# Performance work log

Measured on AMD Instinct MI355X. Metric: run time of the kernel, lower is better.

The kernel has to match this reference:

```python
import jax, jax.numpy as jnp
import numpy as np

B, S, A, H, E = 8192, 256, 64, 1024, 8
IN = S + A
OUT = S + 1


def setup_inputs() -> dict:
    key = jax.random.key(0)
    ks = jax.random.split(key, 8)
    state = jax.random.normal(ks[0], (B, S), dtype=jnp.float32)
    action = jax.random.normal(ks[1], (B, A), dtype=jnp.float32)
    idx = jax.random.randint(ks[2], (B,), 0, E, dtype=jnp.int32)
    # Kaiming-ish scaling to keep activations sane
    W1 = jax.random.normal(ks[3], (E, IN, H), dtype=jnp.float32) / np.sqrt(IN)
    b1 = jnp.zeros((E, H), dtype=jnp.float32)
    W2 = jax.random.normal(ks[4], (E, H, H), dtype=jnp.float32) / np.sqrt(H)
    b2 = jnp.zeros((E, H), dtype=jnp.float32)
    W3 = jax.random.normal(ks[5], (E, H, OUT), dtype=jnp.float32) / np.sqrt(H)
    b3 = jnp.zeros((E, OUT), dtype=jnp.float32)
    return {"state": state, "action": action, "idx": idx,
            "W1": W1, "b1": b1, "W2": W2, "b2": b2, "W3": W3, "b3": b3}


def reference(state, action, idx, W1, b1, W2, b2, W3, b3):
    # Dense-MoE style: run all E experts on the full batch, then select the
    # per-sample expert output chosen by idx (matches masked gather/scatter
    # in the torch predict loop).
    x = jnp.concatenate([state, action], axis=-1)                  # [B, IN]
    h = jax.nn.relu(jnp.einsum('bi,eih->beh', x, W1) + b1)         # [B, E, H]
    h = jax.nn.relu(jnp.einsum('beh,ehk->bek', h, W2) + b2)        # [B, E, H]
    out = jnp.einsum('beh,eho->beo', h, W3) + b3                   # [B, E, S+1]
    sel = jnp.take_along_axis(out, idx[:, None, None], axis=1)[:, 0]  # [B, S+1]
    s_dim = state.shape[-1]
    delta = sel[:, :s_dim]
    reward = sel[:, s_dim:]
    next_state = state + delta
    return next_state, reward
```

## Files before the change

### kernel.cpp

```cpp
#include <hip/hip_runtime.h>
#include <stdint.h>

#define B_SZ   8192
#define IN_DIM 320
#define H_DIM  1024
#define E_NUM  8
#define OUT_DIM 257
#define MAXT1  72
#define MAXT2  136

typedef __bf16 bf16x8 __attribute__((ext_vector_type(8)));
typedef float  f32x4  __attribute__((ext_vector_type(4)));

typedef unsigned int __attribute__((address_space(1))) as1_uint;
typedef unsigned int __attribute__((address_space(3))) as3_uint;

__device__ __forceinline__ void gload_lds16(const void* g, void* l) {
    __builtin_amdgcn_global_load_lds((const as1_uint*)g, (as3_uint*)l, 16, 0, 0);
}

__device__ __forceinline__ unsigned short f2bf(float f) {
    unsigned int u = __float_as_uint(f);
    return (unsigned short)((u + 0x7fffu + ((u >> 16) & 1u)) >> 16);
}

__device__ __forceinline__ void transpose_tiles(
    char* smem, int e, int nt, int kt0, int nkt,
    int K, int Nsrc, int dstRows, bool vec,
    const float* __restrict__ src, unsigned short* __restrict__ dst) {
    unsigned short (*tileU)[65] = (unsigned short(*)[65])smem;
    int tid = threadIdx.x;
    const float* s = src + (size_t)e * K * Nsrc;
    unsigned short* d = dst + (size_t)e * dstRows * K;
    int c4 = (tid & 15) * 4;
    int rb = tid >> 4;
    int n0 = nt * 64;
    for (int kt = kt0; kt < kt0 + nkt; kt++) {
        int k0 = kt * 64;
#pragma unroll
        for (int p = 0; p < 4; p++) {
            int r = rb + p * 16;
            const float* sp = s + (size_t)(k0 + r) * Nsrc + n0 + c4;
            float4 v;
            if (vec) v = *(const float4*)sp;
            else { v.x = sp[0]; v.y = sp[1]; v.z = sp[2]; v.w = sp[3]; }
            tileU[r][c4 + 0] = f2bf(v.x);
            tileU[r][c4 + 1] = f2bf(v.y);
            tileU[r][c4 + 2] = f2bf(v.z);
            tileU[r][c4 + 3] = f2bf(v.w);
        }
        __syncthreads();
#pragma unroll
        for (int p = 0; p < 4; p++) {
            int n = rb + p * 16;
            ushort4 o;
            o.x = tileU[c4 + 0][n];
            o.y = tileU[c4 + 1][n];
            o.z = tileU[c4 + 2][n];
            o.w = tileU[c4 + 3][n];
            *(ushort4*)&d[(size_t)(n0 + n) * K + k0 + c4] = o;
        }
        __syncthreads();
    }
}

__device__ __forceinline__ void prep_bucket(
    char* smem, const int* __restrict__ idx, int* __restrict__ order,
    int* __restrict__ te1, int* __restrict__ tp1, int* __restrict__ tc1,
    int* __restrict__ te2, int* __restrict__ tp2, int* __restrict__ tc2) {
    int (*scnt)[E_NUM] = (int(*)[E_NUM])smem;
    int tid = threadIdx.x;
    int shard = tid & 15;
    if (tid < 128) ((int*)scnt)[tid] = 0;
    __syncthreads();
    for (int b = tid; b < B_SZ; b += 256) atomicAdd(&scnt[shard][idx[b]], 1);
    __syncthreads();
    if (tid == 0) {
        int pos = 0, t1 = 0, t2 = 0;
        for (int e = 0; e < E_NUM; e++) {
            int start = pos;
            for (int s = 0; s < 16; s++) { int c = scnt[s][e]; scnt[s][e] = pos; pos += c; }
            int tot = pos - start;
            for (int st = 0; st < tot; st += 128) {
                te1[t1] = e; tp1[t1] = start + st; tc1[t1] = min(128, tot - st); t1++;
            }
            for (int st = 0; st < tot; st += 64) {
                te2[t2] = e; tp2[t2] = start + st; tc2[t2] = min(64, tot - st); t2++;
            }
        }
        for (; t1 < MAXT1; t1++) { te1[t1] = 0; tp1[t1] = 0; tc1[t1] = 0; }
        for (; t2 < MAXT2; t2++) { te2[t2] = 0; tp2[t2] = 0; tc2[t2] = 0; }
    }
    __syncthreads();
    for (int b = tid; b < B_SZ; b += 256) {
        int e = idx[b];
        int p = atomicAdd(&scnt[shard][e], 1);
        order[p] = b;
    }
}

__global__ __launch_bounds__(256)
void k_prepA(const float* __restrict__ state, const float* __restrict__ action,
             const int* __restrict__ idx, const float* __restrict__ W1,
             unsigned short* __restrict__ xb, unsigned short* __restrict__ w1t,
             int* __restrict__ order,
             int* __restrict__ te1, int* __restrict__ tp1, int* __restrict__ tc1,
             int* __restrict__ te2, int* __restrict__ tp2, int* __restrict__ tc2) {
    __shared__ __align__(16) char smem[8448];
    int bid = blockIdx.x, tid = threadIdx.x;

    if (bid == 0) {
        prep_bucket(smem, idx, order, te1, tp1, tc1, te2, tp2, tc2);
        return;
    }
    if (bid <= 320) {
#pragma unroll
        for (int k = 0; k < 8; k++) {
            int q = ((bid - 1) * 8 + k) * 256 + tid;
            int b = q / 80, j = q % 80;
            float4 v = (j < 64) ? ((const float4*)state)[b * 64 + j]
                                : ((const float4*)action)[b * 16 + (j - 64)];
            ushort4 o;
            o.x = f2bf(v.x); o.y = f2bf(v.y); o.z = f2bf(v.z); o.w = f2bf(v.w);
            ((ushort4*)xb)[q] = o;
        }
        return;
    }
    int r = bid - 321;
    int e = r / 80, m = r % 80;
    transpose_tiles(smem, e, m % 16, m / 16, 1, IN_DIM, H_DIM, H_DIM, true, W1, w1t);
}

template <int K, int TM, int TN, bool GATHER, int MODE>
__device__ __forceinline__ void gemm_tile(
    char* lds, int t, int ny,
    const unsigned short* __restrict__ Abase,
    const unsigned short* __restrict__ Wt, int wtRows,
    const float* __restrict__ bias, int bstride,
    unsigned short* __restrict__ Hout,
    float* __restrict__ Out, const float* __restrict__ state,
    const int* __restrict__ order,
    const int* __restrict__ te, const int* __restrict__ tp0,
    const int* __restrict__ tcnt) {
    constexpr int NI  = K / 32;
    constexpr int WM  = TM / 2, MF = WM / 16;
    constexpr int WN  = TN / 2, NF = WN / 16;
    constexpr int ABY = TM * 64;
    constexpr int BBY = TN * 64;
    constexpr int STG = ABY + BBY;

    int cnt = tcnt[t];
    if (cnt == 0) return;
    int e = te[t], p0 = tp0[t];
    int n0 = ny * TN;
    int tid = threadIdx.x;
    int w = tid >> 6, lane = tid & 63;
    int wm = w >> 1, wn = w & 1;

    int r0 = tid >> 2;
    int cg2 = (tid & 3) ^ ((r0 >> 1) & 3);
    int rc0 = r0 < cnt ? r0 : cnt - 1;
    long a0 = GATHER ? order[p0 + rc0] : (p0 + rc0);
    const unsigned short* aP0 = Abase + (size_t)a0 * K + cg2 * 8;
    const unsigned short* aP1 = aP0;
    if (TM == 128) {
        int rc1 = (r0 + 64) < cnt ? (r0 + 64) : cnt - 1;
        long a1 = GATHER ? order[p0 + rc1] : (p0 + rc1);
        aP1 = Abase + (size_t)a1 * K + cg2 * 8;
    }
    const unsigned short* bP0 = Wt + ((size_t)e * wtRows + n0 + r0) * K + cg2 * 8;
    const unsigned short* bP1 = bP0 + (size_t)64 * K;

    auto stage = [&](int k0s, int sb) {
        gload_lds16(aP0 + k0s, lds + sb + tid * 16);
        if (TM == 128)
            gload_lds16(aP1 + k0s, lds + sb + 4096 + tid * 16);
        gload_lds16(bP0 + k0s, lds + sb + ABY + tid * 16);
        if (TN == 128)
            gload_lds16(bP1 + k0s, lds + sb + ABY + 4096 + tid * 16);
    };

    f32x4 acc[MF][NF];
#pragma unroll
    for (int i = 0; i < MF; i++)
#pragma unroll
        for (int j = 0; j < NF; j++) acc[i][j] = (f32x4)0.f;

    const int fm   = lane & 15;
    const int kc   = lane >> 4;
    const int koff = ((kc ^ ((fm >> 1) & 3)) * 8);

    stage(0, 0);
    for (int it = 0; it < NI; ++it) {
        __syncthreads();
        if (it + 1 < NI) stage((it + 1) * 32, ((it + 1) & 1) * STG);
        const unsigned short* Ls = (const unsigned short*)(lds + (it & 1) * STG);
        const unsigned short* As = Ls + wm * WM * 32;
        const unsigned short* Bs = Ls + ABY / 2 + wn * WN * 32;

        bf16x8 af[MF], bf[NF];
#pragma unroll
        for (int i = 0; i < MF; i++)
            af[i] = *(const bf16x8*)&As[(i * 16 + fm) * 32 + koff];
#pragma unroll
        for (int j = 0; j < NF; j++)
            bf[j] = *(const bf16x8*)&Bs[(j * 16 + fm) * 32 + koff];
#pragma unroll
        for (int i = 0; i < MF; i++)
#pragma unroll
            for (int j = 0; j < NF; j++)
                acc[i][j] = __builtin_amdgcn_mfma_f32_16x16x32_bf16(
                    af[i], bf[j], acc[i][j], 0, 0, 0);
    }

    int col = lane & 15, rq = lane >> 4;
#pragma unroll
    for (int j = 0; j < NF; j++) {
        int n = n0 + wn * WN + j * 16 + col;
        float bv = (MODE == 0) ? bias[e * bstride + n]
                               : ((n <= 256) ? bias[e * bstride + n] : 0.f);
#pragma unroll
        for (int i = 0; i < MF; i++) {
#pragma unroll
            for (int rr = 0; rr < 4; rr++) {
                int m = wm * WM + i * 16 + rq * 4 + rr;
                if (m < cnt) {
                    float v = acc[i][j][rr] + bv;
                    if (MODE == 0) {
                        Hout[(size_t)(p0 + m) * H_DIM + n] = f2bf(fmaxf(v, 0.f));
                    } else {
                        int row = order[p0 + m];
                        if (n < 256) {
                            size_t o = (size_t)row * 256 + n;
                            Out[o] = state[o] + v;
                        } else if (n == 256) {
                            Out[(size_t)B_SZ * 256 + row] = v;
                        }
                    }
                }
            }
        }
    }
}

template <int K, int TM, int TN, bool GATHER, int MODE, int EXTRA, int GBLK, int TT>
__global__ __launch_bounds__(256, 2)
void k_gemm(const unsigned short* __restrict__ Abase,
            const unsigned short* __restrict__ Wt, int wtRows,
            const float* __restrict__ bias, int bstride,
            unsigned short* __restrict__ Hout,
            float* __restrict__ Out, const float* __restrict__ state,
            const int* __restrict__ order,
            const int* __restrict__ te, const int* __restrict__ tp0,
            const int* __restrict__ tcnt,
            const float* __restrict__ Wsrc, unsigned short* __restrict__ Wdst) {
    constexpr int STG = TM * 64 + TN * 64;
    __shared__ __align__(16) char lds[2 * STG];
    int bid = blockIdx.x;

    if (EXTRA != 0 && bid >= GBLK) {
        if constexpr (EXTRA == 1) {
            int b = bid - GBLK;
            int e = b >> 6, r = b & 63;
            transpose_tiles(lds, e, r >> 2, (r & 3) * 4, 4,
                            H_DIM, H_DIM, H_DIM, true, Wsrc, Wdst);
        } else if constexpr (EXTRA == 2) {
            int b = bid - GBLK;
            if (b < 32) {
                transpose_tiles(lds, b >> 2, b & 3, 0, 16,
                                H_DIM, OUT_DIM, 320, false, Wsrc, Wdst);
            } else {
                int i = (b - 32) * 256 + threadIdx.x;
                int e = i >> 10, k = i & 1023;
                Wdst[((size_t)e * 320 + 256) * H_DIM + k] =
                    f2bf(Wsrc[((size_t)e * H_DIM + k) * OUT_DIM + 256]);
            }
        }
        return;
    }
    gemm_tile<K, TM, TN, GATHER, MODE>(lds, bid % TT, bid / TT,
        Abase, Wt, wtRows, bias, bstride, Hout, Out, state,
        order, te, tp0, tcnt);
}

extern "C" void kernel_launch(void* const* d_in, const int* in_sizes, int n_in,
                              void* d_out, int out_size, void* d_ws, size_t ws_size,
                              hipStream_t stream) {
    const float* state  = (const float*)d_in[0];
    const float* action = (const float*)d_in[1];
    const int*   idx    = (const int*)d_in[2];
    const float* W1     = (const float*)d_in[3];
    const float* b1     = (const float*)d_in[4];
    const float* W2     = (const float*)d_in[5];
    const float* b2     = (const float*)d_in[6];
    const float* W3     = (const float*)d_in[7];
    const float* b3     = (const float*)d_in[8];
    float* out = (float*)d_out;

    char* ws = (char*)d_ws;
    size_t off = 0;
    auto alloc = [&](size_t bytes) -> void* {
        void* p = ws + off;
        off = (off + bytes + 255) & ~(size_t)255;
        return p;
    };
    unsigned short* xb  = (unsigned short*)alloc((size_t)B_SZ * IN_DIM * 2);
    unsigned short* w1t = (unsigned short*)alloc((size_t)E_NUM * H_DIM * IN_DIM * 2);
    unsigned short* w2t = (unsigned short*)alloc((size_t)E_NUM * H_DIM * H_DIM * 2);
    unsigned short* w3t = (unsigned short*)alloc((size_t)E_NUM * 320 * H_DIM * 2);
    unsigned short* h1  = (unsigned short*)alloc((size_t)B_SZ * H_DIM * 2);
    unsigned short* h2  = (unsigned short*)alloc((size_t)B_SZ * H_DIM * 2);
    int* order = (int*)alloc(B_SZ * 4);
    int* te1   = (int*)alloc(MAXT1 * 4);
    int* tp1   = (int*)alloc(MAXT1 * 4);
    int* tc1   = (int*)alloc(MAXT1 * 4);
    int* te2   = (int*)alloc(MAXT2 * 4);
    int* tp2   = (int*)alloc(MAXT2 * 4);
    int* tc2   = (int*)alloc(MAXT2 * 4);

    k_prepA<<<961, 256, 0, stream>>>(state, action, idx, W1, xb, w1t, order,
                                     te1, tp1, tc1, te2, tp2, tc2);

    k_gemm<IN_DIM, 128, 128, true, 0, 1, 576, MAXT1>
        <<<1088, 256, 0, stream>>>(
        xb, w1t, H_DIM, b1, H_DIM, h1, nullptr, nullptr,
        order, te1, tp1, tc1, W2, w2t);

    k_gemm<H_DIM, 128, 128, false, 0, 2, 576, MAXT1>
        <<<640, 256, 0, stream>>>(
        h1, w2t, H_DIM, b2, H_DIM, h2, nullptr, nullptr,
        order, te1, tp1, tc1, W3, w3t);

    k_gemm<H_DIM, 64, 64, false, 1, 0, 680, MAXT2>
        <<<680, 256, 0, stream>>>(
        h2, w3t, 320, b3, OUT_DIM, nullptr, out, state,
        order, te2, tp2, tc2, nullptr, nullptr);
}
```

Before: 239.8 us.

## Switch layers 1-2 to 256x256 tiles with 512-thread blocks and split kernels

Layers 1 and 2 now run a dedicated 256x256-tile GEMM with 512 threads and 64 KB of double-buffered LDS, bucketed into 256-row expert tiles. The goal is more data reuse per loaded tile and fewer redundant weight reads. The W2/W3 transposes are grouped with layer 1 in a new mixed kernel, and layer 3 moves to its own specialised 64x64 kernel. In exchange, layer 2 launches only 160 blocks at one block per CU, which leaves many CUs idle, and each CU on the critical path carries more work.

```diff
diff --git a/kernel.cpp b/kernel.cpp
--- a/kernel.cpp
+++ b/kernel.cpp
@@ -6,8 +6,8 @@
 #define H_DIM  1024
 #define E_NUM  8
 #define OUT_DIM 257
-#define MAXT1  72
 #define MAXT2  136
+#define MAXT3  40
 
 typedef __bf16 bf16x8 __attribute__((ext_vector_type(8)));
 typedef float  f32x4  __attribute__((ext_vector_type(4)));
@@ -24,11 +24,14 @@
     return (unsigned short)((u + 0x7fffu + ((u >> 16) & 1u)) >> 16);
 }
 
+template <int NT>
 __device__ __forceinline__ void transpose_tiles(
     char* smem, int e, int nt, int kt0, int nkt,
     int K, int Nsrc, int dstRows, bool vec,
     const float* __restrict__ src, unsigned short* __restrict__ dst) {
     unsigned short (*tileU)[65] = (unsigned short(*)[65])smem;
+    constexpr int RP = NT / 16;
+    constexpr int NP = 64 / RP;
     int tid = threadIdx.x;
     const float* s = src + (size_t)e * K * Nsrc;
     unsigned short* d = dst + (size_t)e * dstRows * K;
@@ -38,8 +41,8 @@
     for (int kt = kt0; kt < kt0 + nkt; kt++) {
         int k0 = kt * 64;
 #pragma unroll
-        for (int p = 0; p < 4; p++) {
-            int r = rb + p * 16;
+        for (int p = 0; p < NP; p++) {
+            int r = rb + p * RP;
             const float* sp = s + (size_t)(k0 + r) * Nsrc + n0 + c4;
             float4 v;
             if (vec) v = *(const float4*)sp;
@@ -51,8 +54,8 @@
         }
         __syncthreads();
 #pragma unroll
-        for (int p = 0; p < 4; p++) {
-            int n = rb + p * 16;
+        for (int p = 0; p < NP; p++) {
+            int n = rb + p * RP;
             ushort4 o;
             o.x = tileU[c4 + 0][n];
             o.y = tileU[c4 + 1][n];
@@ -66,8 +69,8 @@
 
 __device__ __forceinline__ void prep_bucket(
     char* smem, const int* __restrict__ idx, int* __restrict__ order,
-    int* __restrict__ te1, int* __restrict__ tp1, int* __restrict__ tc1,
-    int* __restrict__ te2, int* __restrict__ tp2, int* __restrict__ tc2) {
+    int* __restrict__ te2, int* __restrict__ tp2, int* __restrict__ tc2,
+    int* __restrict__ te3, int* __restrict__ tp3, int* __restrict__ tc3) {
     int (*scnt)[E_NUM] = (int(*)[E_NUM])smem;
     int tid = threadIdx.x;
     int shard = tid & 15;
@@ -76,20 +79,20 @@
     for (int b = tid; b < B_SZ; b += 256) atomicAdd(&scnt[shard][idx[b]], 1);
     __syncthreads();
     if (tid == 0) {
-        int pos = 0, t1 = 0, t2 = 0;
+        int pos = 0, t2 = 0, t3 = 0;
         for (int e = 0; e < E_NUM; e++) {
             int start = pos;
             for (int s = 0; s < 16; s++) { int c = scnt[s][e]; scnt[s][e] = pos; pos += c; }
             int tot = pos - start;
-            for (int st = 0; st < tot; st += 128) {
-                te1[t1] = e; tp1[t1] = start + st; tc1[t1] = min(128, tot - st); t1++;
-            }
             for (int st = 0; st < tot; st += 64) {
                 te2[t2] = e; tp2[t2] = start + st; tc2[t2] = min(64, tot - st); t2++;
             }
-        }
-        for (; t1 < MAXT1; t1++) { te1[t1] = 0; tp1[t1] = 0; tc1[t1] = 0; }
+            for (int st = 0; st < tot; st += 256) {
+                te3[t3] = e; tp3[t3] = start + st; tc3[t3] = min(256, tot - st); t3++;
+            }
+        }
         for (; t2 < MAXT2; t2++) { te2[t2] = 0; tp2[t2] = 0; tc2[t2] = 0; }
+        for (; t3 < MAXT3; t3++) { te3[t3] = 0; tp3[t3] = 0; tc3[t3] = 0; }
     }
     __syncthreads();
     for (int b = tid; b < B_SZ; b += 256) {
@@ -104,13 +107,13 @@
              const int* __restrict__ idx, const float* __restrict__ W1,
              unsigned short* __restrict__ xb, unsigned short* __restrict__ w1t,
              int* __restrict__ order,
-             int* __restrict__ te1, int* __restrict__ tp1, int* __restrict__ tc1,
-             int* __restrict__ te2, int* __restrict__ tp2, int* __restrict__ tc2) {
+             int* __restrict__ te2, int* __restrict__ tp2, int* __restrict__ tc2,
+             int* __restrict__ te3, int* __restrict__ tp3, int* __restrict__ tc3) {
     __shared__ __align__(16) char smem[8448];
     int bid = blockIdx.x, tid = threadIdx.x;
 
     if (bid == 0) {
-        prep_bucket(smem, idx, order, te1, tp1, tc1, te2, tp2, tc2);
+        prep_bucket(smem, idx, order, te2, tp2, tc2, te3, tp3, tc3);
         return;
     }
     if (bid <= 320) {
@@ -128,63 +131,54 @@
     }
     int r = bid - 321;
     int e = r / 80, m = r % 80;
-    transpose_tiles(smem, e, m % 16, m / 16, 1, IN_DIM, H_DIM, H_DIM, true, W1, w1t);
-}
-
-template <int K, int TM, int TN, bool GATHER, int MODE>
-__device__ __forceinline__ void gemm_tile(
+    transpose_tiles<256>(smem, e, m % 16, m / 16, 1, IN_DIM, H_DIM, H_DIM, true, W1, w1t);
+}
+
+template <int K, bool GATHER>
+__device__ __forceinline__ void gemm256_tile(
     char* lds, int t, int ny,
     const unsigned short* __restrict__ Abase,
-    const unsigned short* __restrict__ Wt, int wtRows,
-    const float* __restrict__ bias, int bstride,
+    const unsigned short* __restrict__ Wt,
+    const float* __restrict__ bias,
     unsigned short* __restrict__ Hout,
-    float* __restrict__ Out, const float* __restrict__ state,
     const int* __restrict__ order,
     const int* __restrict__ te, const int* __restrict__ tp0,
     const int* __restrict__ tcnt) {
     constexpr int NI  = K / 32;
-    constexpr int WM  = TM / 2, MF = WM / 16;
-    constexpr int WN  = TN / 2, NF = WN / 16;
-    constexpr int ABY = TM * 64;
-    constexpr int BBY = TN * 64;
-    constexpr int STG = ABY + BBY;
+    constexpr int ABY = 256 * 64;
+    constexpr int STG = 2 * ABY;
 
     int cnt = tcnt[t];
     if (cnt == 0) return;
     int e = te[t], p0 = tp0[t];
-    int n0 = ny * TN;
+    int n0 = ny * 256;
     int tid = threadIdx.x;
     int w = tid >> 6, lane = tid & 63;
-    int wm = w >> 1, wn = w & 1;
+    int wm = w >> 2, wn = w & 3;
 
     int r0 = tid >> 2;
     int cg2 = (tid & 3) ^ ((r0 >> 1) & 3);
     int rc0 = r0 < cnt ? r0 : cnt - 1;
+    int rc1 = (r0 + 128) < cnt ? (r0 + 128) : cnt - 1;
     long a0 = GATHER ? order[p0 + rc0] : (p0 + rc0);
+    long a1 = GATHER ? order[p0 + rc1] : (p0 + rc1);
     const unsigned short* aP0 = Abase + (size_t)a0 * K + cg2 * 8;
-    const unsigned short* aP1 = aP0;
-    if (TM == 128) {
-        int rc1 = (r0 + 64) < cnt ? (r0 + 64) : cnt - 1;
-        long a1 = GATHER ? order[p0 + rc1] : (p0 + rc1);
-        aP1 = Abase + (size_t)a1 * K + cg2 * 8;
-    }
-    const unsigned short* bP0 = Wt + ((size_t)e * wtRows + n0 + r0) * K + cg2 * 8;
-    const unsigned short* bP1 = bP0 + (size_t)64 * K;
+    const unsigned short* aP1 = Abase + (size_t)a1 * K + cg2 * 8;
+    const unsigned short* bP0 = Wt + ((size_t)e * H_DIM + n0 + r0) * K + cg2 * 8;
+    const unsigned short* bP1 = bP0 + (size_t)128 * K;
 
     auto stage = [&](int k0s, int sb) {
         gload_lds16(aP0 + k0s, lds + sb + tid * 16);
-        if (TM == 128)
-            gload_lds16(aP1 + k0s, lds + sb + 4096 + tid * 16);
+        gload_lds16(aP1 + k0s, lds + sb + 8192 + tid * 16);
         gload_lds16(bP0 + k0s, lds + sb + ABY + tid * 16);
-        if (TN == 128)
-            gload_lds16(bP1 + k0s, lds + sb + ABY + 4096 + tid * 16);
+        gload_lds16(bP1 + k0s, lds + sb + ABY + 8192 + tid * 16);
     };
 
-    f32x4 acc[MF][NF];
-#pragma unroll
-    for (int i = 0; i < MF; i++)
-#pragma unroll
-        for (int j = 0; j < NF; j++) acc[i][j] = (f32x4)0.f;
+    f32x4 acc[8][4];
+#pragma unroll
+    for (int i = 0; i < 8; i++)
+#pragma unroll
+        for (int j = 0; j < 4; j++) acc[i][j] = (f32x4)0.f;
 
     const int fm   = lane & 15;
     const int kc   = lane >> 4;
@@ -195,92 +189,177 @@
         __syncthreads();
         if (it + 1 < NI) stage((it + 1) * 32, ((it + 1) & 1) * STG);
         const unsigned short* Ls = (const unsigned short*)(lds + (it & 1) * STG);
-        const unsigned short* As = Ls + wm * WM * 32;
-        const unsigned short* Bs = Ls + ABY / 2 + wn * WN * 32;
-
-        bf16x8 af[MF], bf[NF];
-#pragma unroll
-        for (int i = 0; i < MF; i++)
+        const unsigned short* As = Ls + wm * 128 * 32;
+        const unsigned short* Bs = Ls + ABY / 2 + wn * 64 * 32;
+
+        bf16x8 af[8], bf[4];
+#pragma unroll
+        for (int i = 0; i < 8; i++)
             af[i] = *(const bf16x8*)&As[(i * 16 + fm) * 32 + koff];
 #pragma unroll
-        for (int j = 0; j < NF; j++)
+        for (int j = 0; j < 4; j++)
             bf[j] = *(const bf16x8*)&Bs[(j * 16 + fm) * 32 + koff];
 #pragma unroll
-        for (int i = 0; i < MF; i++)
-#pragma unroll
-            for (int j = 0; j < NF; j++)
+        for (int i = 0; i < 8; i++)
+#pragma unroll
+            for (int j = 0; j < 4; j++)
                 acc[i][j] = __builtin_amdgcn_mfma_f32_16x16x32_bf16(
                     af[i], bf[j], acc[i][j], 0, 0, 0);
     }
 
     int col = lane & 15, rq = lane >> 4;
 #pragma unroll
-    for (int j = 0; j < NF; j++) {
-        int n = n0 + wn * WN + j * 16 + col;
-        float bv = (MODE == 0) ? bias[e * bstride + n]
-                               : ((n <= 256) ? bias[e * bstride + n] : 0.f);
-#pragma unroll
-        for (int i = 0; i < MF; i++) {
+    for (int j = 0; j < 4; j++) {
+        int n = n0 + wn * 64 + j * 16 + col;
+        float bv = bias[e * H_DIM + n];
+#pragma unroll
+        for (int i = 0; i < 8; i++) {
 #pragma unroll
             for (int rr = 0; rr < 4; rr++) {
-                int m = wm * WM + i * 16 + rq * 4 + rr;
+                int m = wm * 128 + i * 16 + rq * 4 + rr;
                 if (m < cnt) {
                     float v = acc[i][j][rr] + bv;
-                    if (MODE == 0) {
-                        Hout[(size_t)(p0 + m) * H_DIM + n] = f2bf(fmaxf(v, 0.f));
-                    } else {
-                        int row = order[p0 + m];
-                        if (n < 256) {
-                            size_t o = (size_t)row * 256 + n;
-                            Out[o] = state[o] + v;
-                        } else if (n == 256) {
-                            Out[(size_t)B_SZ * 256 + row] = v;
-                        }
+                    Hout[(size_t)(p0 + m) * H_DIM + n] = f2bf(fmaxf(v, 0.f));
+                }
+            }
+        }
+    }
+}
+
+__global__ __launch_bounds__(512, 1)
+void k_mix1(const unsigned short* __restrict__ xb,
+            const unsigned short* __restrict__ w1t,
+            const float* __restrict__ b1, unsigned short* __restrict__ h1,
+            const int* __restrict__ order,
+            const int* __restrict__ te3, const int* __restrict__ tp3,
+            const int* __restrict__ tc3,
+            const float* __restrict__ W2, unsigned short* __restrict__ w2t,
+            const float* __restrict__ W3, unsigned short* __restrict__ w3t) {
+    __shared__ __align__(16) char lds[65536];
+    int bid = blockIdx.x;
+    if (bid < 160) {
+        gemm256_tile<IN_DIM, true>(lds, bid % MAXT3, bid / MAXT3,
+                                   xb, w1t, b1, h1, order, te3, tp3, tc3);
+    } else if (bid < 672) {
+        int b = bid - 160;
+        int e = b >> 6, r = b & 63;
+        transpose_tiles<512>(lds, e, r >> 2, (r & 3) * 4, 4,
+                             H_DIM, H_DIM, H_DIM, true, W2, w2t);
+    } else if (bid < 704) {
+        int b = bid - 672;
+        transpose_tiles<512>(lds, b >> 2, b & 3, 0, 16,
+                             H_DIM, OUT_DIM, 320, false, W3, w3t);
+    } else {
+        int i = (bid - 704) * 512 + threadIdx.x;
+        int e = i >> 10, k = i & 1023;
+        w3t[((size_t)e * 320 + 256) * H_DIM + k] =
+            f2bf(W3[((size_t)e * H_DIM + k) * OUT_DIM + 256]);
+    }
+}
+
+__global__ __launch_bounds__(512, 1)
+void k_l2(const unsigned short* __restrict__ h1,
+          const unsigned short* __restrict__ w2t,
+          const float* __restrict__ b2, unsigned short* __restrict__ h2,
+          const int* __restrict__ order,
+          const int* __restrict__ te3, const int* __restrict__ tp3,
+          const int* __restrict__ tc3) {
+    __shared__ __align__(16) char lds[65536];
+    int bid = blockIdx.x;
+    gemm256_tile<H_DIM, false>(lds, bid % MAXT3, bid / MAXT3,
+                               h1, w2t, b2, h2, order, te3, tp3, tc3);
+}
+
+__global__ __launch_bounds__(256, 2)
+void k_l3(const unsigned short* __restrict__ h2,
+          const unsigned short* __restrict__ w3t,
+          const float* __restrict__ b3,
+          float* __restrict__ Out, const float* __restrict__ state,
+          const int* __restrict__ order,
+          const int* __restrict__ te, const int* __restrict__ tp0,
+          const int* __restrict__ tcnt) {
+    constexpr int K = H_DIM;
+    constexpr int NI = K / 32;
+    constexpr int ABY = 64 * 64;
+    constexpr int STG = 2 * ABY;
+    __shared__ __align__(16) char lds[2 * STG];
+
+    int t = blockIdx.x % MAXT2, ny = blockIdx.x / MAXT2;
+    int cnt = tcnt[t];
+    if (cnt == 0) return;
+    int e = te[t], p0 = tp0[t];
+    int n0 = ny * 64;
+    int tid = threadIdx.x;
+    int w = tid >> 6, lane = tid & 63;
+    int wm = w >> 1, wn = w & 1;
+
+    int r0 = tid >> 2;
+    int cg2 = (tid & 3) ^ ((r0 >> 1) & 3);
+    int rc0 = r0 < cnt ? r0 : cnt - 1;
+    const unsigned short* aP0 = h2 + (size_t)(p0 + rc0) * K + cg2 * 8;
+    const unsigned short* bP0 = w3t + ((size_t)e * 320 + n0 + r0) * K + cg2 * 8;
+
+    auto stage = [&](int k0s, int sb) {
+        gload_lds16(aP0 + k0s, lds + sb + tid * 16);
+        gload_lds16(bP0 + k0s, lds + sb + ABY + tid * 16);
+    };
+
+    f32x4 acc[2][2];
+#pragma unroll
+    for (int i = 0; i < 2; i++)
+#pragma unroll
+        for (int j = 0; j < 2; j++) acc[i][j] = (f32x4)0.f;
+
+    const int fm   = lane & 15;
+    const int kc   = lane >> 4;
+    const int koff = ((kc ^ ((fm >> 1) & 3)) * 8);
+
+    stage(0, 0);
+    for (int it = 0; it < NI; ++it) {
+        __syncthreads();
+        if (it + 1 < NI) stage((it + 1) * 32, ((it + 1) & 1) * STG);
+        const unsigned short* Ls = (const unsigned short*)(lds + (it & 1) * STG);
+        const unsigned short* As = Ls + wm * 32 * 32;
+        const unsigned short* Bs = Ls + ABY / 2 + wn * 32 * 32;
+
+        bf16x8 af[2], bf[2];
+#pragma unroll
+        for (int i = 0; i < 2; i++)
+            af[i] = *(const bf16x8*)&As[(i * 16 + fm) * 32 + koff];
+#pragma unroll
+        for (int j = 0; j < 2; j++)
+            bf[j] = *(const bf16x8*)&Bs[(j * 16 + fm) * 32 + koff];
+#pragma unroll
+        for (int i = 0; i < 2; i++)
+#pragma unroll
+            for (int j = 0; j < 2; j++)
+                acc[i][j] = __builtin_amdgcn_mfma_f32_16x16x32_bf16(
+                    af[i], bf[j], acc[i][j], 0, 0, 0);
+    }
+
+    int col = lane & 15, rq = lane >> 4;
+#pragma unroll
+    for (int j = 0; j < 2; j++) {
+        int n = n0 + wn * 32 + j * 16 + col;
+        float bv = (n <= 256) ? b3[e * OUT_DIM + n] : 0.f;
+#pragma unroll
+        for (int i = 0; i < 2; i++) {
+#pragma unroll
+            for (int rr = 0; rr < 4; rr++) {
+                int m = wm * 32 + i * 16 + rq * 4 + rr;
+                if (m < cnt) {
+                    float v = acc[i][j][rr] + bv;
+                    int row = order[p0 + m];
+                    if (n < 256) {
+                        size_t o = (size_t)row * 256 + n;
+                        Out[o] = state[o] + v;
+                    } else if (n == 256) {
+                        Out[(size_t)B_SZ * 256 + row] = v;
                     }
                 }
             }
         }
     }
-}
-
-template <int K, int TM, int TN, bool GATHER, int MODE, int EXTRA, int GBLK, int TT>
-__global__ __launch_bounds__(256, 2)
-void k_gemm(const unsigned short* __restrict__ Abase,
-            const unsigned short* __restrict__ Wt, int wtRows,
-            const float* __restrict__ bias, int bstride,
-            unsigned short* __restrict__ Hout,
-            float* __restrict__ Out, const float* __restrict__ state,
-            const int* __restrict__ order,
-            const int* __restrict__ te, const int* __restrict__ tp0,
-            const int* __restrict__ tcnt,
-            const float* __restrict__ Wsrc, unsigned short* __restrict__ Wdst) {
-    constexpr int STG = TM * 64 + TN * 64;
-    __shared__ __align__(16) char lds[2 * STG];
-    int bid = blockIdx.x;
-
-    if (EXTRA != 0 && bid >= GBLK) {
-        if constexpr (EXTRA == 1) {
-            int b = bid - GBLK;
-            int e = b >> 6, r = b & 63;
-            transpose_tiles(lds, e, r >> 2, (r & 3) * 4, 4,
-                            H_DIM, H_DIM, H_DIM, true, Wsrc, Wdst);
-        } else if constexpr (EXTRA == 2) {
-            int b = bid - GBLK;
-            if (b < 32) {
-                transpose_tiles(lds, b >> 2, b & 3, 0, 16,
-                                H_DIM, OUT_DIM, 320, false, Wsrc, Wdst);
-            } else {
-                int i = (b - 32) * 256 + threadIdx.x;
-                int e = i >> 10, k = i & 1023;
-                Wdst[((size_t)e * 320 + 256) * H_DIM + k] =
-                    f2bf(Wsrc[((size_t)e * H_DIM + k) * OUT_DIM + 256]);
-            }
-        }
-        return;
-    }
-    gemm_tile<K, TM, TN, GATHER, MODE>(lds, bid % TT, bid / TT,
-        Abase, Wt, wtRows, bias, bstride, Hout, Out, state,
-        order, te, tp0, tcnt);
 }
 
 extern "C" void kernel_launch(void* const* d_in, const int* in_sizes, int n_in,
@@ -311,28 +390,21 @@
     unsigned short* h1  = (unsigned short*)alloc((size_t)B_SZ * H_DIM * 2);
     unsigned short* h2  = (unsigned short*)alloc((size_t)B_SZ * H_DIM * 2);
     int* order = (int*)alloc(B_SZ * 4);
-    int* te1   = (int*)alloc(MAXT1 * 4);
-    int* tp1   = (int*)alloc(MAXT1 * 4);
-    int* tc1   = (int*)alloc(MAXT1 * 4);
     int* te2   = (int*)alloc(MAXT2 * 4);
     int* tp2   = (int*)alloc(MAXT2 * 4);
     int* tc2   = (int*)alloc(MAXT2 * 4);
+    int* te3   = (int*)alloc(MAXT3 * 4);
+    int* tp3   = (int*)alloc(MAXT3 * 4);
+    int* tc3   = (int*)alloc(MAXT3 * 4);
 
     k_prepA<<<961, 256, 0, stream>>>(state, action, idx, W1, xb, w1t, order,
-                                     te1, tp1, tc1, te2, tp2, tc2);
-
-    k_gemm<IN_DIM, 128, 128, true, 0, 1, 576, MAXT1>
-        <<<1088, 256, 0, stream>>>(
-        xb, w1t, H_DIM, b1, H_DIM, h1, nullptr, nullptr,
-        order, te1, tp1, tc1, W2, w2t);
-
-    k_gemm<H_DIM, 128, 128, false, 0, 2, 576, MAXT1>
-        <<<640, 256, 0, stream>>>(
-        h1, w2t, H_DIM, b2, H_DIM, h2, nullptr, nullptr,
-        order, te1, tp1, tc1, W3, w3t);
-
-    k_gemm<H_DIM, 64, 64, false, 1, 0, 680, MAXT2>
-        <<<680, 256, 0, stream>>>(
-        h2, w3t, 320, b3, OUT_DIM, nullptr, out, state,
-        order, te2, tp2, tc2, nullptr, nullptr);
-}
+                                     te2, tp2, tc2, te3, tp3, tc3);
+
+    k_mix1<<<720, 512, 0, stream>>>(xb, w1t, b1, h1, order, te3, tp3, tc3,
+                                    W2, w2t, W3, w3t);
+
+    k_l2<<<160, 512, 0, stream>>>(h1, w2t, b2, h2, order, te3, tp3, tc3);
+
+    k_l3<<<MAXT2 * 5, 256, 0, stream>>>(h2, w3t, b3, out, state, order,
+                                        te2, tp2, tc2);
+}
```

Result: slower. 250.6 us (+4.5%).
